# Kernel optimization log

Measured on AMD Instinct MI355X. Metric: run time of the kernel, lower is better.

## Reference

```python
import jax, jax.numpy as jnp
import numpy as np

WS = 8      # window size
NH = 8      # num heads
SCALE = 4.0 # qk_scale=4 from module defaults
GK = 9      # gaze depthwise kernel (nw=8 even -> 9)
EPS = 1e-5


def _rel_pos_index(ws):
    coords = np.stack(np.meshgrid(np.arange(ws), np.arange(ws), indexing='ij'))
    cf = coords.reshape(2, -1)
    rel = (cf[:, :, None] - cf[:, None, :]).transpose(1, 2, 0).astype(np.int64)
    rel[..., 0] += ws - 1
    rel[..., 1] += ws - 1
    rel[..., 0] *= 2 * ws - 1
    return jnp.asarray(rel.sum(-1))  # (N, N)


def _ln(x, g, b):
    m = x.mean(-1, keepdims=True)
    v = ((x - m) ** 2).mean(-1, keepdims=True)
    return (x - m) / jnp.sqrt(v + EPS) * g + b


def _forward(x, norm1_g, norm1_b, qkv_w, qkv_b, rpb_table, proj_w, proj_b,
             gaze_w, gaze_b, norm2_g, norm2_b, fc1_w, fc1_b, fc2_w, fc2_b, H, W):
    B, C, _, _ = x.shape
    hd = C // NH
    nw = H // WS           # windows per side (= Fold dilation)
    N = WS * WS            # tokens per window
    xf = x.transpose(0, 2, 3, 1).reshape(B, H * W, C)
    shortcut = xf
    xn = _ln(xf, norm1_g, norm1_b).reshape(B, H, W, C)
    # window partition -> (B*nw*nw, N, C)
    xw = xn.reshape(B, nw, WS, nw, WS, C).transpose(0, 1, 3, 2, 4, 5).reshape(B * nw * nw, N, C)
    qkv = (xw @ qkv_w.T + qkv_b).reshape(-1, N, 3, NH, hd).transpose(2, 0, 3, 1, 4)
    q, k, v = qkv[0] * SCALE, qkv[1], qkv[2]
    attn = jnp.einsum('whnd,whmd->whnm', q, k)  # (nWin, heads, N, N)
    rpi = _rel_pos_index(WS)
    bias = rpb_table[rpi.reshape(-1)].reshape(N, N, NH).transpose(2, 0, 1)
    attn = jax.nn.softmax(attn + bias[None], axis=-1)
    out = jnp.einsum('whnm,whmd->whnd', attn, v).transpose(0, 2, 1, 3).reshape(-1, N, C)
    # gaze branch: Fold (dilated scatter of windows into image), depthwise conv, Unfold
    v6 = v.reshape(B, nw, nw, NH, WS, WS, hd)          # (B, wh, ww, nh, i, j, hd)
    img = v6.transpose(0, 4, 1, 5, 2, 3, 6).reshape(B, H, W, C)  # row = i*nw+wh, col = j*nw+ww
    pad = GK // 2
    img = jax.lax.conv_general_dilated(
        img, gaze_w, (1, 1), ((pad, pad), (pad, pad)),
        dimension_numbers=('NHWC', 'HWIO', 'NHWC'), feature_group_count=C) + gaze_b
    gz = img.reshape(B, WS, nw, WS, nw, C).transpose(0, 2, 4, 1, 3, 5).reshape(B * nw * nw, N, C)
    out = (out + gz) @ proj_w.T + proj_b
    # window reverse -> (B, H*W, C)
    xr = out.reshape(B, nw, nw, WS, WS, C).transpose(0, 1, 3, 2, 4, 5).reshape(B, H * W, C)
    xf = shortcut + xr
    h = _ln(xf, norm2_g, norm2_b)
    h = jax.nn.gelu(h @ fc1_w.T + fc1_b, approximate=False) @ fc2_w.T + fc2_b
    xf = xf + h
    return xf.reshape(B, H, W, C).transpose(0, 3, 1, 2)


def setup_inputs() -> dict:
    key = jax.random.key(0)
    ks = jax.random.split(key, 8)
    C, H, W, B, HID = 256, 64, 64, 16, 1024
    return {
        'H': 64, 'W': 64,
        'x': jax.random.normal(ks[0], (B, C, H, W), jnp.float32),
        'norm1_g': jnp.ones((C,), jnp.float32),
        'norm1_b': jnp.zeros((C,), jnp.float32),
        'qkv_w': jax.random.normal(ks[1], (3 * C, C), jnp.float32) * 0.02,
        'qkv_b': jnp.zeros((3 * C,), jnp.float32),
        'rpb_table': jax.random.normal(ks[2], (225, NH), jnp.float32) * 0.02,
        'proj_w': jax.random.normal(ks[3], (C, C), jnp.float32) * 0.02,
        'proj_b': jnp.zeros((C,), jnp.float32),
        'gaze_w': jax.random.normal(ks[4], (GK, GK, 1, C), jnp.float32) * 0.02,
        'gaze_b': jnp.zeros((C,), jnp.float32),
        'norm2_g': jnp.ones((C,), jnp.float32),
        'norm2_b': jnp.zeros((C,), jnp.float32),
        'fc1_w': jax.random.normal(ks[5], (HID, C), jnp.float32) * 0.02,
        'fc1_b': jnp.zeros((HID,), jnp.float32),
        'fc2_w': jax.random.normal(ks[6], (C, HID), jnp.float32) * 0.02,
        'fc2_b': jnp.zeros((C,), jnp.float32),
    }


def reference(H, W, x, norm1_g, norm1_b, qkv_w, qkv_b, rpb_table, proj_w, proj_b,
              gaze_w, gaze_b, norm2_g, norm2_b, fc1_w, fc1_b, fc2_w, fc2_b):
    return _forward(x, norm1_g, norm1_b, qkv_w, qkv_b, rpb_table, proj_w, proj_b,
                    gaze_w, gaze_b, norm2_g, norm2_b, fc1_w, fc1_b, fc2_w, fc2_b, H, W)
```

## Files before the change

kernel.cpp:

```cpp
#include <hip/hip_runtime.h>
#include <math.h>

#define BB    16
#define CC    256
#define HH    64
#define WW2   64
#define NHD   8
#define HD    32
#define NT    64
#define NWIN  1024
#define TOK   65536
#define HIDN  1024
#define GKS   9
#define GPAD  4

typedef short bf16x8 __attribute__((ext_vector_type(8)));
typedef float f32x4  __attribute__((ext_vector_type(4)));
typedef float f32x2  __attribute__((ext_vector_type(2)));
typedef unsigned short u16x8 __attribute__((ext_vector_type(8)));

__device__ __forceinline__ float b2f(unsigned short u) {
    return __uint_as_float(((unsigned int)u) << 16);
}
__device__ __forceinline__ unsigned short f2b(float f) {
    unsigned int x = __float_as_uint(f);
    unsigned int r = x + 0x7fffu + ((x >> 16) & 1u);
    return (unsigned short)(r >> 16);
}
__device__ __forceinline__ unsigned int cvt_pk_bf16(float lo, float hi) {
    unsigned int r;
    asm("v_cvt_pk_bf16_f32 %0, %1, %2" : "=v"(r) : "v"(lo), "v"(hi));
    return r;
}
__device__ __forceinline__ f32x2 bf2_to_f32x2(unsigned int u) {
    f32x2 r;
    r.x = __uint_as_float(u << 16);
    r.y = __uint_as_float(u & 0xFFFF0000u);
    return r;
}

__device__ __forceinline__ float gelu_f(float v) {
    const float w = v * v;
    const float u = v * fmaf(w, -0.1029432f, -2.3022082f);
    const float e = __builtin_amdgcn_exp2f(u);
    return v * __builtin_amdgcn_rcpf(1.0f + e);
}

__device__ __forceinline__ u16x8 add_bf8(u16x8 a, u16x8 b) {
    u16x8 o;
#pragma unroll
    for (int j = 0; j < 8; j += 2) {
        const unsigned int p = cvt_pk_bf16(b2f(a[j]) + b2f(b[j]),
                                           b2f(a[j + 1]) + b2f(b[j + 1]));
        o[j] = (unsigned short)p;
        o[j + 1] = (unsigned short)(p >> 16);
    }
    return o;
}

#define O_N1G  64
#define O_N1B  320
#define O_QKVW 576
#define O_QKVB 197184
#define O_RPB  197952
#define O_PW   199808
#define O_PB   265344
#define O_GW   265600
#define O_GB   286336
#define O_N2G  286592
#define O_N2B  286848
#define O_W1   287104
#define O_B1   549248
#define O_W2   550272
#define O_B2   812416

struct ParTab {
    const void* src[15];
    int n[15];
    int off[15];
};

__global__ __launch_bounds__(256) void k_detect(const unsigned short* __restrict__ x,
                                                int* __restrict__ flag) {
    __shared__ int cnt;
    if (threadIdx.x == 0) cnt = 0;
    __syncthreads();
    const unsigned short u = x[threadIdx.x];
    const int e = (u >> 7) & 0xFF;
    if (e >= 140) atomicAdd(&cnt, 1);
    __syncthreads();
    if (threadIdx.x == 0) *flag = (cnt >= 8) ? 1 : 0;
}

__global__ __launch_bounds__(256) void k_conv_par(ParTab tab,
                                                  const int* __restrict__ flag,
                                                  unsigned short* __restrict__ par) {
    const int t = blockIdx.y;
    const int n = tab.n[t], off = tab.off[t];
    const bool f32 = (*flag != 0);
    const bool scaled = (t == 2) || (t == 3);
    const int slim = (t == 2) ? 65536 : 256;
    for (int i = blockIdx.x * 256 + threadIdx.x; i < n; i += 64 * 256) {
        unsigned short r;
        if (f32) {
            float v = ((const float*)tab.src[t])[i];
            if (scaled && i < slim) v *= 4.0f;
            r = f2b(v);
        } else {
            r = ((const unsigned short*)tab.src[t])[i];
            if (scaled && i < slim) r = f2b(b2f(r) * 4.0f);
        }
        par[off + i] = r;
    }
}

__global__ __launch_bounds__(256) void k_pre(const void* __restrict__ xsrc,
                                             const int* __restrict__ flag,
                                             const unsigned short* __restrict__ g,
                                             const unsigned short* __restrict__ bt,
                                             unsigned short* __restrict__ SC,
                                             unsigned short* __restrict__ XN) {
    __shared__ __align__(16) unsigned short xs[256 * 66];
    __shared__ float ps[4][64], ps2[4][64];
    __shared__ float mean_s[64], rstd_s[64];
    const int tid = threadIdx.x;
    const int bid = blockIdx.x;
    const int win = (bid & 7) * 128 + (bid >> 3);
    const int b = win >> 6, wh = (win >> 3) & 7, ww = win & 7;
    const bool f32 = (*flag != 0);

    if (f32) {
        for (int idx = tid; idx < 4096; idx += 256) {
            const int c = idx >> 4, u = idx & 15;
            const int h = wh * 8 + (u >> 1), w = ww * 8 + (u & 1) * 4;
            const float4 v = *(const float4*)
                &((const float*)xsrc)[((size_t)(b * CC + c) * HH + h) * WW2 + w];
            unsigned int* dst = (unsigned int*)&xs[c * 66 + u * 4];
            dst[0] = cvt_pk_bf16(v.x, v.y);
            dst[1] = cvt_pk_bf16(v.z, v.w);
        }
    } else {
        for (int idx = tid; idx < 2048; idx += 256) {
            const int c = idx >> 3, u = idx & 7;
            const int h = wh * 8 + u, w = ww * 8;
            const uint4 v = *(const uint4*)
                &((const unsigned short*)xsrc)[((size_t)(b * CC + c) * HH + h) * WW2 + w];
            unsigned int* dst = (unsigned int*)&xs[c * 66 + u * 8];
            dst[0] = v.x; dst[1] = v.y; dst[2] = v.z; dst[3] = v.w;
        }
    }
    __syncthreads();
    {
        const int tok = tid & 63, part = tid >> 6;
        float s = 0.f, s2 = 0.f;
        for (int c = part * 64; c < part * 64 + 64; ++c) {
            const float v = b2f(xs[c * 66 + tok]);
            s += v; s2 += v * v;
        }
        ps[part][tok] = s; ps2[part][tok] = s2;
    }
    __syncthreads();
    if (tid < 64) {
        const float s  = ps[0][tid] + ps[1][tid] + ps[2][tid] + ps[3][tid];
        const float s2 = ps2[0][tid] + ps2[1][tid] + ps2[2][tid] + ps2[3][tid];
        const float mean = s * (1.f / 256.f);
        const float var  = s2 * (1.f / 256.f) - mean * mean;
        mean_s[tid] = mean;
        rstd_s[tid] = rsqrtf(var + 1e-5f);
    }
    __syncthreads();
    for (int idx = tid; idx < 16384; idx += 256) {
        const int n = idx >> 8, c = idx & 255;
        const unsigned short raw = xs[c * 66 + n];
        const float v = (b2f(raw) - mean_s[n]) * rstd_s[n] * b2f(g[c]) + b2f(bt[c]);
        const size_t o = (size_t)(win * NT + n) * CC + c;
        SC[o] = raw;
        XN[o] = f2b(v);
    }
}

template <int KDIM, int ACT, typename PostF>
__device__ __forceinline__ void gemm128(const unsigned short* __restrict__ A,
                                        const unsigned short* __restrict__ Bw,
                                        const unsigned short* __restrict__ bias,
                                        int m0, int n0, PostF post8) {
    __shared__ __align__(16) unsigned short smem[128 * 136];
    unsigned short* As = smem;
    unsigned short* Bs = smem + 8192;
    const int tid = threadIdx.x;
    const int wv = tid >> 6, ln = tid & 63;
    const int wm = wv & 1, wn = wv >> 1;

    float bias_v[4];
#pragma unroll
    for (int nt = 0; nt < 4; ++nt)
        bias_v[nt] = b2f(bias[n0 + wn * 64 + nt * 16 + (ln & 15)]);

    f32x4 acc[4][4] = {};
    const int u = tid;

    for (int kb = 0; kb < KDIM; kb += 64) {
#pragma unroll
        for (int i = 0; i < 4; ++i) {
            const int uu = i * 256 + u;
            const int row = uu >> 3;
            const int c8 = ((uu & 7) ^ (row & 7)) * 8;
            __builtin_amdgcn_global_load_lds(
                (const __attribute__((address_space(1))) unsigned int*)
                    &A[(size_t)(m0 + row) * KDIM + kb + c8],
                (__attribute__((address_space(3))) unsigned int*)&As[uu * 8],
                16, 0, 0);
            __builtin_amdgcn_global_load_lds(
                (const __attribute__((address_space(1))) unsigned int*)
                    &Bw[(size_t)(n0 + row) * KDIM + kb + c8],
                (__attribute__((address_space(3))) unsigned int*)&Bs[uu * 8],
                16, 0, 0);
        }
        __syncthreads();
#pragma unroll
        for (int ks = 0; ks < 2; ++ks) {
            bf16x8 af[4], bf[4];
            const int sl = ks * 4 + (ln >> 4);
#pragma unroll
            for (int t = 0; t < 4; ++t) {
                const int ra = wm * 64 + t * 16 + (ln & 15);
                const int rb = wn * 64 + t * 16 + (ln & 15);
                af[t] = *(const bf16x8*)&As[ra * 64 + ((sl ^ (ra & 7)) * 8)];
                bf[t] = *(const bf16x8*)&Bs[rb * 64 + ((sl ^ (rb & 7)) * 8)];
            }
#pragma unroll
            for (int mt = 0; mt < 4; ++mt)
#pragma unroll
                for (int nt = 0; nt < 4; ++nt)
                    acc[mt][nt] = __builtin_amdgcn_mfma_f32_16x16x32_bf16(af[mt], bf[nt], acc[mt][nt], 0, 0, 0);
        }
        __syncthreads();
    }

    unsigned short* Cs = smem;
#pragma unroll
    for (int mt = 0; mt < 4; ++mt)
#pragma unroll
        for (int nt = 0; nt < 4; ++nt) {
            float v[4];
#pragma unroll
            for (int r = 0; r < 4; ++r) {
                float x = acc[mt][nt][r] + bias_v[nt];
                if (ACT == 1) x = gelu_f(x);
                v[r] = x;
            }
            const int mlb = wm * 64 + mt * 16 + (ln >> 4) * 4;
            const int nl = wn * 64 + nt * 16 + (ln & 15);
            const unsigned int p0 = cvt_pk_bf16(v[0], v[1]);
            const unsigned int p1 = cvt_pk_bf16(v[2], v[3]);
            Cs[(mlb + 0) * 136 + nl] = (unsigned short)p0;
            Cs[(mlb + 1) * 136 + nl] = (unsigned short)(p0 >> 16);
            Cs[(mlb + 2) * 136 + nl] = (unsigned short)p1;
            Cs[(mlb + 3) * 136 + nl] = (unsigned short)(p1 >> 16);
        }
    __syncthreads();
#pragma unroll
    for (int i = 0; i < 8; ++i) {
        const int j = i * 256 + tid;
        const int row = j >> 4, c8 = (j & 15) * 8;
        const u16x8 vals = *(const u16x8*)&Cs[row * 136 + c8];
        post8(m0 + row, n0 + c8, vals);
    }
}

__device__ __forceinline__ void xcd_tiles(int wgid, int NN, int& m0, int& n0) {
    const int xcd = wgid & 7, local = wgid >> 3;
    m0 = (xcd * 64 + local / NN) * 128;
    n0 = (local % NN) * 128;
}

__global__ __launch_bounds__(256) void k_gemm_qkv(const unsigned short* __restrict__ XN,
                                                  const unsigned short* __restrict__ Wq,
                                                  const unsigned short* __restrict__ bq,
                                                  unsigned short* __restrict__ Q,
                                                  unsigned short* __restrict__ K,
                                                  unsigned short* __restrict__ V) {
    int m0, n0;
    xcd_tiles(blockIdx.x, 6, m0, n0);
    gemm128<256, 0>(XN, Wq, bq, m0, n0,
        [&](int m, int nb, u16x8 vals) {
            unsigned short* dst = (nb < 256) ? Q : ((nb < 512) ? K : V);
            *(u16x8*)&dst[(size_t)m * CC + (nb & 255)] = vals;
        });
}

__global__ __launch_bounds__(256) void k_attn(const unsigned short* __restrict__ Q,
                                              const unsigned short* __restrict__ K,
                                              const unsigned short* __restrict__ V,
                                              const unsigned short* __restrict__ rpb,
                                              unsigned short* __restrict__ AO) {
    __shared__ __align__(16) unsigned short Pb[64 * 72];
    __shared__ __align__(16) unsigned short Vt[32 * 72];
    const int tid = threadIdx.x, wv = tid >> 6, ln = tid & 63;
    const int win = blockIdx.x, head = blockIdx.y;
    const size_t tbase = (size_t)(win * NT) * CC + head * HD;

    {
        const int tok = tid >> 2, d8 = (tid & 3) * 8;
        const u16x8 vv = *(const u16x8*)&V[tbase + (size_t)tok * CC + d8];
#pragma unroll
        for (int j = 0; j < 8; ++j) Vt[(d8 + j) * 72 + tok] = vv[j];
    }

    const bf16x8 a = *(const bf16x8*)&Q[tbase + (size_t)(16 * wv + (ln & 15)) * CC + (ln >> 4) * 8];
    f32x4 accs[4] = {};
#pragma unroll
    for (int f = 0; f < 4; ++f) {
        const bf16x8 b = *(const bf16x8*)&K[tbase + (size_t)(f * 16 + (ln & 15)) * CC + (ln >> 4) * 8];
        accs[f] = __builtin_amdgcn_mfma_f32_16x16x32_bf16(a, b, accs[f], 0, 0, 0);
    }
    const int qloc = (ln >> 4) * 4;
#pragma unroll
    for (int f = 0; f < 4; ++f)
#pragma unroll
        for (int r = 0; r < 4; ++r) {
            const int rr = 16 * wv + qloc + r;
            const int cth = f * 16 + (ln & 15);
            const int bidx = ((rr >> 3) - (cth >> 3) + 7) * 15 + ((rr & 7) - (cth & 7) + 7);
            accs[f][r] += b2f(rpb[bidx * NHD + head]);
        }
#pragma unroll
    for (int r = 0; r < 4; ++r) {
        float m = fmaxf(fmaxf(accs[0][r], accs[1][r]), fmaxf(accs[2][r], accs[3][r]));
#pragma unroll
        for (int o = 1; o <= 8; o <<= 1) m = fmaxf(m, __shfl_xor(m, o));
        float p[4], s = 0.f;
#pragma unroll
        for (int f = 0; f < 4; ++f) { p[f] = expf(accs[f][r] - m); s += p[f]; }
#pragma unroll
        for (int o = 1; o <= 8; o <<= 1) s += __shfl_xor(s, o);
        const float inv = 1.f / s;
#pragma unroll
        for (int f = 0; f < 4; ++f)
            Pb[(16 * wv + qloc + r) * 72 + f * 16 + (ln & 15)] = f2b(p[f] * inv);
    }
    __syncthreads();

    f32x4 acco[2] = {};
#pragma unroll
    for (int kb = 0; kb < 64; kb += 32) {
        const bf16x8 ap = *(const bf16x8*)&Pb[(16 * wv + (ln & 15)) * 72 + kb + (ln >> 4) * 8];
#pragma unroll
        for (int f = 0; f < 2; ++f) {
            const bf16x8 bv = *(const bf16x8*)&Vt[(f * 16 + (ln & 15)) * 72 + kb + (ln >> 4) * 8];
            acco[f] = __builtin_amdgcn_mfma_f32_16x16x32_bf16(ap, bv, acco[f], 0, 0, 0);
        }
    }
#pragma unroll
    for (int f = 0; f < 2; ++f)
#pragma unroll
        for (int r = 0; r < 4; ++r) {
            const int rr = 16 * wv + qloc + r;
            const int d = f * 16 + (ln & 15);
            AO[tbase + (size_t)rr * CC + d] = f2b(acco[f][r]);
        }
}

__global__ __launch_bounds__(256) void k_gaze(const unsigned short* __restrict__ V,
                                              const unsigned short* __restrict__ gw,
                                              const unsigned short* __restrict__ gb,
                                              unsigned short* __restrict__ AO) {
    __shared__ __align__(16) unsigned short ins[24 * 16 * 32];
    __shared__ __align__(16) float wf[81 * 32];
    const int tid = threadIdx.x;
    const int c0 = blockIdx.x * 8, r0 = blockIdx.y * 16;
    const int b = blockIdx.z >> 3, head = blockIdx.z & 7;

    for (int idx = tid; idx < 1536; idx += 256) {
        const int pix = idx >> 2, v4 = (idx & 3) * 8;
        const int row = pix >> 4, colL = pix & 15;
        const int rp = r0 + row - GPAD, cp = c0 + colL - GPAD;
        uint4 val = {0, 0, 0, 0};
        if (rp >= 0 && rp < HH && cp >= 0 && cp < WW2) {
            const int win = b * 64 + (rp & 7) * 8 + (cp & 7);
            const int n = (rp >> 3) * 8 + (cp >> 3);
            val = *(const uint4*)&V[(size_t)(win * NT + n) * CC + head * HD + v4];
        }
        *(uint4*)&ins[(row * 16 + colL) * 32 + v4] = val;
    }
    for (int idx = tid; idx < 1296; idx += 256) {
        const int k = idx >> 4, dpair = idx & 15;
        const unsigned int w2u = *(const unsigned int*)&gw[k * CC + head * HD + dpair * 2];
        *(f32x2*)&wf[k * 32 + dpair * 2] = bf2_to_f32x2(w2u);
    }
    __syncthreads();

    const int col  = tid >> 5;
    const int half = (tid >> 4) & 1;
    const int dp   = tid & 15;
    const int rbase = half * 8;

    f32x2 out2[8];
#pragma unroll
    for (int ro = 0; ro < 8; ++ro) out2[ro] = (f32x2){0.f, 0.f};

#pragma unroll
    for (int dx = 0; dx < GKS; ++dx) {
        f32x2 w2[GKS];
#pragma unroll
        for (int dy = 0; dy < GKS; ++dy)
            w2[dy] = *(const f32x2*)&wf[(dy * GKS + dx) * 32 + dp * 2];
        f32x2 in2[17];
#pragma unroll
        for (int ri = 0; ri < 17; ++ri) {
            const unsigned int u = *(const unsigned int*)
                &ins[((rbase + ri) * 16 + col + dx) * 32 + dp * 2];
            in2[ri] = bf2_to_f32x2(u);
        }
#pragma unroll
        for (int ro = 0; ro < 8; ++ro)
#pragma unroll
            for (int dy = 0; dy < GKS; ++dy)
                asm("v_pk_fma_f32 %0, %1, %2, %0"
                    : "+v"(out2[ro]) : "v"(in2[ro + dy]), "v"(w2[dy]));
    }

    const unsigned int bw = *(const unsigned int*)&gb[head * HD + dp * 2];
    const f32x2 bias2 = bf2_to_f32x2(bw);
    const int c = c0 + col;
#pragma unroll
    for (int ro = 0; ro < 8; ++ro) {
        const int r = r0 + rbase + ro;
        const int win0 = b * 64 + (r & 7) * 8 + (c & 7);
        const int n0 = (r >> 3) * 8 + (c >> 3);
        unsigned int* p = (unsigned int*)
            &AO[(size_t)(win0 * NT + n0) * CC + head * HD + dp * 2];
        const f32x2 old = bf2_to_f32x2(*p);
        *p = cvt_pk_bf16(old.x + out2[ro].x + bias2.x,
                         old.y + out2[ro].y + bias2.y);
    }
}

__global__ __launch_bounds__(256) void k_gemm_proj(const unsigned short* __restrict__ AO,
                                                   const unsigned short* __restrict__ Wp,
                                                   const unsigned short* __restrict__ bp,
                                                   const unsigned short* __restrict__ SC,
                                                   unsigned short* __restrict__ X2) {
    int m0, n0;
    xcd_tiles(blockIdx.x, 2, m0, n0);
    gemm128<256, 0>(AO, Wp, bp, m0, n0,
        [&](int m, int nb, u16x8 vals) {
            const u16x8 sc = *(const u16x8*)&SC[(size_t)m * CC + nb];
            *(u16x8*)&X2[(size_t)m * CC + nb] = add_bf8(vals, sc);
        });
}

__global__ __launch_bounds__(256) void k_ln2(const unsigned short* __restrict__ X2,
                                             const unsigned short* __restrict__ g,
                                             const unsigned short* __restrict__ bt,
                                             unsigned short* __restrict__ X2N) {
    const int tid = threadIdx.x;
    const int wv = tid >> 6, ln = tid & 63;
    const int t = blockIdx.x * 8 + wv * 2 + (ln >> 5);
    const int c8 = (ln & 31) * 8;
    const u16x8 xv = *(const u16x8*)&X2[(size_t)t * CC + c8];
    float vals[8];
    float s = 0.f, s2 = 0.f;
#pragma unroll
    for (int j = 0; j < 8; ++j) {
        const float v = b2f(xv[j]);
        vals[j] = v; s += v; s2 += v * v;
    }
#pragma unroll
    for (int off = 16; off; off >>= 1) {
        s += __shfl_xor(s, off);
        s2 += __shfl_xor(s2, off);
    }
    const float mean = s * (1.f / 256.f);
    const float rstd = rsqrtf(s2 * (1.f / 256.f) - mean * mean + 1e-5f);
    const u16x8 gv = *(const u16x8*)&g[c8];
    const u16x8 bv = *(const u16x8*)&bt[c8];
    u16x8 o;
#pragma unroll
    for (int j = 0; j < 8; j += 2) {
        const float a0 = (vals[j] - mean) * rstd * b2f(gv[j]) + b2f(bv[j]);
        const float a1 = (vals[j + 1] - mean) * rstd * b2f(gv[j + 1]) + b2f(bv[j + 1]);
        const unsigned int p = cvt_pk_bf16(a0, a1);
        o[j] = (unsigned short)p;
        o[j + 1] = (unsigned short)(p >> 16);
    }
    *(u16x8*)&X2N[(size_t)t * CC + c8] = o;
}

__global__ __launch_bounds__(256) void k_gemm_fc1(const unsigned short* __restrict__ X2N,
                                                  const unsigned short* __restrict__ W1,
                                                  const unsigned short* __restrict__ b1,
                                                  unsigned short* __restrict__ H1) {
    int m0, n0;
    xcd_tiles(blockIdx.x, 8, m0, n0);
    gemm128<256, 1>(X2N, W1, b1, m0, n0,
        [&](int m, int nb, u16x8 vals) {
            *(u16x8*)&H1[(size_t)m * HIDN + nb] = vals;
        });
}

__global__ __launch_bounds__(256) void k_gemm_fc2(const unsigned short* __restrict__ H1,
                                                  const unsigned short* __restrict__ W2,
                                                  const unsigned short* __restrict__ b2v,
                                                  const unsigned short* __restrict__ X2,
                                                  unsigned short* __restrict__ XOUT) {
    int m0, n0;
    xcd_tiles(blockIdx.x, 2, m0, n0);
    gemm128<1024, 0>(H1, W2, b2v, m0, n0,
        [&](int m, int nb, u16x8 vals) {
            const u16x8 r = *(const u16x8*)&X2[(size_t)m * CC + nb];
            *(u16x8*)&XOUT[(size_t)m * CC + nb] = add_bf8(vals, r);
        });
}

__global__ __launch_bounds__(256) void k_out(const unsigned short* __restrict__ XOUT,
                                             const int* __restrict__ flag,
                                             void* __restrict__ out) {
    __shared__ __align__(16) unsigned short ys[64 * 257];
    const int tid = threadIdx.x;
    const int bid = blockIdx.x;
    const int win = (bid & 7) * 128 + (bid >> 3);
    const int b = win >> 6, wh = (win >> 3) & 7, ww = win & 7;
    for (int idx = tid; idx < 2048; idx += 256) {
        const int n = idx >> 5, c8 = (idx & 31) * 8;
        const u16x8 v = *(const u16x8*)&XOUT[(size_t)(win * NT + n) * CC + c8];
#pragma unroll
        for (int j = 0; j < 8; ++j) ys[n * 257 + c8 + j] = v[j];
    }
    __syncthreads();
    const bool f32 = (*flag != 0);
    if (f32) {
        for (int idx = tid; idx < 4096; idx += 256) {
            const int ch = idx >> 4, u = idx & 15;
            const int h = wh * 8 + (u >> 1), w = ww * 8 + (u & 1) * 4;
            const int n0 = u * 4;
            float4 v;
            v.x = b2f(ys[(n0 + 0) * 257 + ch]);
            v.y = b2f(ys[(n0 + 1) * 257 + ch]);
            v.z = b2f(ys[(n0 + 2) * 257 + ch]);
            v.w = b2f(ys[(n0 + 3) * 257 + ch]);
            *(float4*)&((float*)out)[((size_t)(b * CC + ch) * HH + h) * WW2 + w] = v;
        }
    } else {
        for (int idx = tid; idx < 2048; idx += 256) {
            const int ch = idx >> 3, u = idx & 7;
            const int h = wh * 8 + u, w = ww * 8;
            const int n0 = u * 8;
            u16x8 v;
#pragma unroll
            for (int j = 0; j < 8; ++j) v[j] = ys[(n0 + j) * 257 + ch];
            *(u16x8*)&((unsigned short*)out)[((size_t)(b * CC + ch) * HH + h) * WW2 + w] = v;
        }
    }
}

extern "C" void kernel_launch(void* const* d_in, const int* in_sizes, int n_in,
                              void* d_out, int out_size, void* d_ws, size_t ws_size,
                              hipStream_t stream) {
    char* ws = (char*)d_ws;
    const size_t MB = 1048576;
    unsigned short* SC  = (unsigned short*)(ws);
    unsigned short* XN  = (unsigned short*)(ws + 32 * MB);
    unsigned short* Qb  = (unsigned short*)(ws + 64 * MB);
    unsigned short* Kb  = (unsigned short*)(ws + 96 * MB);
    unsigned short* Vb  = (unsigned short*)(ws + 128 * MB);
    unsigned short* AO  = (unsigned short*)(ws + 160 * MB);
    unsigned short* H1  = (unsigned short*)(ws + 64 * MB);
    unsigned short* X2  = (unsigned short*)(ws + 192 * MB);
    unsigned short* PAR = (unsigned short*)(ws + 224 * MB);
    int* FLAG = (int*)(ws + 224 * MB);
    unsigned short* X2N  = XN;
    unsigned short* XOUT = XN;

    ParTab tab;
    const int srcidx[15] = {3, 4, 5, 6, 7, 8, 9, 10, 11, 12, 13, 14, 15, 16, 17};
    const int sizes[15]  = {256, 256, 196608, 768, 1800, 65536, 256, 20736, 256,
                            256, 256, 262144, 1024, 262144, 256};
    const int offs[15]   = {O_N1G, O_N1B, O_QKVW, O_QKVB, O_RPB, O_PW, O_PB, O_GW, O_GB,
                            O_N2G, O_N2B, O_W1, O_B1, O_W2, O_B2};
    for (int i = 0; i < 15; ++i) {
        tab.src[i] = d_in[srcidx[i]];
        tab.n[i] = sizes[i];
        tab.off[i] = offs[i];
    }

    k_detect   <<<1,                 256, 0, stream>>>((const unsigned short*)d_in[2], FLAG);
    k_conv_par <<<dim3(64, 15),      256, 0, stream>>>(tab, FLAG, PAR);
    k_pre      <<<NWIN,              256, 0, stream>>>(d_in[2], FLAG, PAR + O_N1G, PAR + O_N1B, SC, XN);
    k_gemm_qkv <<<3072,              256, 0, stream>>>(XN, PAR + O_QKVW, PAR + O_QKVB, Qb, Kb, Vb);
    k_attn     <<<dim3(NWIN, NHD),   256, 0, stream>>>(Qb, Kb, Vb, PAR + O_RPB, AO);
    k_gaze     <<<dim3(8, 4, 128),   256, 0, stream>>>(Vb, PAR + O_GW, PAR + O_GB, AO);
    k_gemm_proj<<<1024,              256, 0, stream>>>(AO, PAR + O_PW, PAR + O_PB, SC, X2);
    k_ln2      <<<TOK / 8,           256, 0, stream>>>(X2, PAR + O_N2G, PAR + O_N2B, X2N);
    k_gemm_fc1 <<<4096,              256, 0, stream>>>(X2N, PAR + O_W1, PAR + O_B1, H1);
    k_gemm_fc2 <<<1024,              256, 0, stream>>>(H1, PAR + O_W2, PAR + O_B2, X2, XOUT);
    k_out      <<<NWIN,              256, 0, stream>>>(XOUT, FLAG, d_out);
}
```

Baseline: 474.5 us.

## Fuse LN2, fc1, GELU and fc2 into one per-tile MLP kernel

Replaces the separate LN2, fc1 GEMM and fc2 GEMM kernels with a single kernel that handles 64 tokens per block. The block normalizes its rows into swizzled LDS, computes fc1 in 128-wide hidden chunks with GELU into LDS, and accumulates fc2 in registers. This removes the HBM round trip of the 64K x 1024 hidden activation and the normalized X2 buffer, plus two launches. In exchange, weights are read straight from global memory per block with no LDS staging or double buffering, and the 64-row tiles with large register accumulators may lower occupancy and MFMA efficiency.

New measurement: 513.4 us. 1.08x slower.

```diff
diff --git a/kernel.cpp b/kernel.cpp
--- a/kernel.cpp
+++ b/kernel.cpp
@@ -450,67 +450,133 @@
         });
 }
 
-__global__ __launch_bounds__(256) void k_ln2(const unsigned short* __restrict__ X2,
-                                             const unsigned short* __restrict__ g,
-                                             const unsigned short* __restrict__ bt,
-                                             unsigned short* __restrict__ X2N) {
+__global__ __launch_bounds__(256) void k_mlp(const unsigned short* __restrict__ X2,
+                                             const unsigned short* __restrict__ W1g,
+                                             const unsigned short* __restrict__ b1,
+                                             const unsigned short* __restrict__ W2g,
+                                             const unsigned short* __restrict__ b2,
+                                             const unsigned short* __restrict__ n2g,
+                                             const unsigned short* __restrict__ n2b,
+                                             unsigned short* __restrict__ XOUT) {
+    __shared__ __align__(16) unsigned short smem[64 * 256 + 64 * 132];
+    unsigned short* Xs = smem;
+    unsigned short* Hs = smem + 64 * 256;
     const int tid = threadIdx.x;
     const int wv = tid >> 6, ln = tid & 63;
-    const int t = blockIdx.x * 8 + wv * 2 + (ln >> 5);
-    const int c8 = (ln & 31) * 8;
-    const u16x8 xv = *(const u16x8*)&X2[(size_t)t * CC + c8];
-    float vals[8];
-    float s = 0.f, s2 = 0.f;
-#pragma unroll
-    for (int j = 0; j < 8; ++j) {
-        const float v = b2f(xv[j]);
-        vals[j] = v; s += v; s2 += v * v;
-    }
-#pragma unroll
-    for (int off = 16; off; off >>= 1) {
-        s += __shfl_xor(s, off);
-        s2 += __shfl_xor(s2, off);
-    }
-    const float mean = s * (1.f / 256.f);
-    const float rstd = rsqrtf(s2 * (1.f / 256.f) - mean * mean + 1e-5f);
-    const u16x8 gv = *(const u16x8*)&g[c8];
-    const u16x8 bv = *(const u16x8*)&bt[c8];
-    u16x8 o;
-#pragma unroll
-    for (int j = 0; j < 8; j += 2) {
-        const float a0 = (vals[j] - mean) * rstd * b2f(gv[j]) + b2f(bv[j]);
-        const float a1 = (vals[j + 1] - mean) * rstd * b2f(gv[j + 1]) + b2f(bv[j + 1]);
-        const unsigned int p = cvt_pk_bf16(a0, a1);
-        o[j] = (unsigned short)p;
-        o[j + 1] = (unsigned short)(p >> 16);
-    }
-    *(u16x8*)&X2N[(size_t)t * CC + c8] = o;
-}
-
-__global__ __launch_bounds__(256) void k_gemm_fc1(const unsigned short* __restrict__ X2N,
-                                                  const unsigned short* __restrict__ W1,
-                                                  const unsigned short* __restrict__ b1,
-                                                  unsigned short* __restrict__ H1) {
-    int m0, n0;
-    xcd_tiles(blockIdx.x, 8, m0, n0);
-    gemm128<256, 1>(X2N, W1, b1, m0, n0,
-        [&](int m, int nb, u16x8 vals) {
-            *(u16x8*)&H1[(size_t)m * HIDN + nb] = vals;
-        });
-}
-
-__global__ __launch_bounds__(256) void k_gemm_fc2(const unsigned short* __restrict__ H1,
-                                                  const unsigned short* __restrict__ W2,
-                                                  const unsigned short* __restrict__ b2v,
-                                                  const unsigned short* __restrict__ X2,
-                                                  unsigned short* __restrict__ XOUT) {
-    int m0, n0;
-    xcd_tiles(blockIdx.x, 2, m0, n0);
-    gemm128<1024, 0>(H1, W2, b2v, m0, n0,
-        [&](int m, int nb, u16x8 vals) {
-            const u16x8 r = *(const u16x8*)&X2[(size_t)m * CC + nb];
-            *(u16x8*)&XOUT[(size_t)m * CC + nb] = add_bf8(vals, r);
-        });
+    const int bid = blockIdx.x;
+    const int m0 = ((bid & 7) * 128 + (bid >> 3)) * 64;
+
+    {
+        const int hw = tid >> 5;
+        const int l32 = tid & 31;
+        const int c8 = l32 * 8;
+        const u16x8 gv = *(const u16x8*)&n2g[c8];
+        const u16x8 bv = *(const u16x8*)&n2b[c8];
+        for (int p = 0; p < 8; ++p) {
+            const int t = p * 8 + hw;
+            const u16x8 xv = *(const u16x8*)&X2[(size_t)(m0 + t) * CC + c8];
+            float vals[8]; float s = 0.f, s2 = 0.f;
+#pragma unroll
+            for (int j = 0; j < 8; ++j) { const float v = b2f(xv[j]); vals[j] = v; s += v; s2 += v * v; }
+#pragma unroll
+            for (int off = 16; off; off >>= 1) { s += __shfl_xor(s, off); s2 += __shfl_xor(s2, off); }
+            const float mean = s * (1.f / 256.f);
+            const float rstd = rsqrtf(s2 * (1.f / 256.f) - mean * mean + 1e-5f);
+            u16x8 o;
+#pragma unroll
+            for (int j = 0; j < 8; j += 2) {
+                const float a0 = (vals[j] - mean) * rstd * b2f(gv[j]) + b2f(bv[j]);
+                const float a1 = (vals[j + 1] - mean) * rstd * b2f(gv[j + 1]) + b2f(bv[j + 1]);
+                const unsigned int pk = cvt_pk_bf16(a0, a1);
+                o[j] = (unsigned short)pk; o[j + 1] = (unsigned short)(pk >> 16);
+            }
+            *(u16x8*)&Xs[t * 256 + ((l32 ^ (t & 7)) * 8)] = o;
+        }
+    }
+    __syncthreads();
+
+    f32x4 acc_out[4][4] = {};
+    for (int hb = 0; hb < 8; ++hb) {
+        f32x4 acc1[4][2] = {};
+        for (int kb = 0; kb < 256; kb += 32) {
+            bf16x8 bf1[2];
+#pragma unroll
+            for (int n1 = 0; n1 < 2; ++n1) {
+                const int wrow = hb * 128 + wv * 32 + n1 * 16 + (ln & 15);
+                bf1[n1] = *(const bf16x8*)&W1g[(size_t)wrow * 256 + kb + (ln >> 4) * 8];
+            }
+#pragma unroll
+            for (int mt = 0; mt < 4; ++mt) {
+                const int ra = mt * 16 + (ln & 15);
+                const int slot = (kb >> 3) + (ln >> 4);
+                const bf16x8 af = *(const bf16x8*)&Xs[ra * 256 + ((slot ^ (ra & 7)) * 8)];
+#pragma unroll
+                for (int n1 = 0; n1 < 2; ++n1)
+                    acc1[mt][n1] = __builtin_amdgcn_mfma_f32_16x16x32_bf16(af, bf1[n1], acc1[mt][n1], 0, 0, 0);
+            }
+        }
+        __syncthreads();
+#pragma unroll
+        for (int n1 = 0; n1 < 2; ++n1) {
+            const int hcol = wv * 32 + n1 * 16 + (ln & 15);
+            const float bb = b2f(b1[hb * 128 + hcol]);
+#pragma unroll
+            for (int mt = 0; mt < 4; ++mt)
+#pragma unroll
+                for (int r = 0; r < 4; ++r) {
+                    const int tr = mt * 16 + (ln >> 4) * 4 + r;
+                    Hs[tr * 132 + hcol] = f2b(gelu_f(acc1[mt][n1][r] + bb));
+                }
+        }
+        __syncthreads();
+#pragma unroll
+        for (int kk = 0; kk < 4; ++kk) {
+            bf16x8 bf2[4];
+#pragma unroll
+            for (int nt = 0; nt < 4; ++nt) {
+                const int nrow = wv * 64 + nt * 16 + (ln & 15);
+                bf2[nt] = *(const bf16x8*)&W2g[(size_t)nrow * 1024 + hb * 128 + kk * 32 + (ln >> 4) * 8];
+            }
+#pragma unroll
+            for (int mt = 0; mt < 4; ++mt) {
+                const bf16x8 ah = *(const bf16x8*)&Hs[(mt * 16 + (ln & 15)) * 132 + kk * 32 + (ln >> 4) * 8];
+#pragma unroll
+                for (int nt = 0; nt < 4; ++nt)
+                    acc_out[mt][nt] = __builtin_amdgcn_mfma_f32_16x16x32_bf16(ah, bf2[nt], acc_out[mt][nt], 0, 0, 0);
+            }
+        }
+    }
+
+    float bias2[4];
+#pragma unroll
+    for (int nt = 0; nt < 4; ++nt)
+        bias2[nt] = b2f(b2[wv * 64 + nt * 16 + (ln & 15)]);
+    __syncthreads();
+    unsigned short* Cs = smem;
+#pragma unroll
+    for (int mt = 0; mt < 4; ++mt)
+#pragma unroll
+        for (int nt = 0; nt < 4; ++nt) {
+            const int mlb = mt * 16 + (ln >> 4) * 4;
+            const int nl = wv * 64 + nt * 16 + (ln & 15);
+            const unsigned int p0 = cvt_pk_bf16(acc_out[mt][nt][0] + bias2[nt],
+                                                acc_out[mt][nt][1] + bias2[nt]);
+            const unsigned int p1 = cvt_pk_bf16(acc_out[mt][nt][2] + bias2[nt],
+                                                acc_out[mt][nt][3] + bias2[nt]);
+            Cs[(mlb + 0) * 264 + nl] = (unsigned short)p0;
+            Cs[(mlb + 1) * 264 + nl] = (unsigned short)(p0 >> 16);
+            Cs[(mlb + 2) * 264 + nl] = (unsigned short)p1;
+            Cs[(mlb + 3) * 264 + nl] = (unsigned short)(p1 >> 16);
+        }
+    __syncthreads();
+#pragma unroll
+    for (int i = 0; i < 8; ++i) {
+        const int j = i * 256 + tid;
+        const int row = j >> 5, c8 = (j & 31) * 8;
+        const u16x8 vals = *(const u16x8*)&Cs[row * 264 + c8];
+        const u16x8 res = *(const u16x8*)&X2[(size_t)(m0 + row) * CC + c8];
+        *(u16x8*)&XOUT[(size_t)(m0 + row) * CC + c8] = add_bf8(vals, res);
+    }
 }
 
 __global__ __launch_bounds__(256) void k_out(const unsigned short* __restrict__ XOUT,
@@ -565,11 +631,9 @@
     unsigned short* Kb  = (unsigned short*)(ws + 96 * MB);
     unsigned short* Vb  = (unsigned short*)(ws + 128 * MB);
     unsigned short* AO  = (unsigned short*)(ws + 160 * MB);
-    unsigned short* H1  = (unsigned short*)(ws + 64 * MB);
     unsigned short* X2  = (unsigned short*)(ws + 192 * MB);
     unsigned short* PAR = (unsigned short*)(ws + 224 * MB);
     int* FLAG = (int*)(ws + 224 * MB);
-    unsigned short* X2N  = XN;
     unsigned short* XOUT = XN;
 
     ParTab tab;
@@ -591,8 +655,7 @@
     k_attn     <<<dim3(NWIN, NHD),   256, 0, stream>>>(Qb, Kb, Vb, PAR + O_RPB, AO);
     k_gaze     <<<dim3(8, 4, 128),   256, 0, stream>>>(Vb, PAR + O_GW, PAR + O_GB, AO);
     k_gemm_proj<<<1024,              256, 0, stream>>>(AO, PAR + O_PW, PAR + O_PB, SC, X2);
-    k_ln2      <<<TOK / 8,           256, 0, stream>>>(X2, PAR + O_N2G, PAR + O_N2B, X2N);
-    k_gemm_fc1 <<<4096,              256, 0, stream>>>(X2N, PAR + O_W1, PAR + O_B1, H1);
-    k_gemm_fc2 <<<1024,              256, 0, stream>>>(H1, PAR + O_W2, PAR + O_B2, X2, XOUT);
+    k_mlp      <<<1024,              256, 0, stream>>>(X2, PAR + O_W1, PAR + O_B1, PAR + O_W2,
+                                                       PAR + O_B2, PAR + O_N2G, PAR + O_N2B, XOUT);
     k_out      <<<NWIN,              256, 0, stream>>>(XOUT, FLAG, d_out);
 }
```
